# Kernel tuning notes

Hardware: AMD Instinct MI355X
Metric: run time of the kernel (lower is better)

## Reference

```python
import jax, jax.numpy as jnp
import numpy as np

B, T, D = 2, 1024, 768
H, HS = 12, 64          # n_head, head_size = n_embed // n_head
E, K = 8, 1             # num_experts, top-k (MoeLayer default k=1)
DF = 4 * D              # FFN hidden
EPS = 1e-5


def _ln(x, g, b):
    mu = jnp.mean(x, axis=-1, keepdims=True)
    var = jnp.mean(jnp.square(x - mu), axis=-1, keepdims=True)
    return (x - mu) * jax.lax.rsqrt(var + EPS) * g + b


def setup_inputs() -> dict:
    key = jax.random.key(0)
    ks = jax.random.split(key, 12)
    s = 0.02
    return {
        "x": jax.random.normal(ks[0], (B, T, D), dtype=jnp.float32),
        "ln1_g": jnp.ones((D,), jnp.float32),
        "ln1_b": jnp.zeros((D,), jnp.float32),
        "ln2_g": jnp.ones((D,), jnp.float32),
        "ln2_b": jnp.zeros((D,), jnp.float32),
        "Wq": jax.random.normal(ks[1], (H, D, HS), jnp.float32) * s,
        "Wk": jax.random.normal(ks[2], (H, D, HS), jnp.float32) * s,
        "Wv": jax.random.normal(ks[3], (H, D, HS), jnp.float32) * s,
        "Wp": jax.random.normal(ks[4], (D, D), jnp.float32) * s,
        "bp": jnp.zeros((D,), jnp.float32),
        "Wg": jax.random.normal(ks[5], (D, E), jnp.float32) * s,
        "W1": jax.random.normal(ks[6], (E, D, DF), jnp.float32) * s,
        "b1": jnp.zeros((E, DF), jnp.float32),
        "W2": jax.random.normal(ks[7], (E, DF, D), jnp.float32) * s,
        "b2": jnp.zeros((E, D), jnp.float32),
    }


def reference(x, ln1_g, ln1_b, ln2_g, ln2_b, Wq, Wk, Wv, Wp, bp, Wg, W1, b1, W2, b2):
    b, t, d = x.shape

    # ---- multi-head causal self-attention (per-head QKV, as in Head) ----
    h = _ln(x, ln1_g, ln1_b)
    q = jnp.einsum('btd,hds->bhts', h, Wq)
    k = jnp.einsum('btd,hds->bhts', h, Wk)
    v = jnp.einsum('btd,hds->bhts', h, Wv)
    # NOTE: original scales by C**-0.5 with C = n_embed (not head_size)
    scores = jnp.einsum('bhts,bhus->bhtu', q, k) * (d ** -0.5)
    causal = jnp.tril(jnp.ones((t, t), dtype=bool))
    scores = jnp.where(causal, scores, -jnp.inf)
    att = jax.nn.softmax(scores, axis=-1)
    out = jnp.einsum('bhtu,bhus->bhts', att, v)          # [B,H,T,HS]
    out = out.transpose(0, 2, 1, 3).reshape(b, t, d)     # concat heads
    x = x + out @ Wp + bp

    # ---- top-k MoE feed-forward (MoeLayer, k=1) ----
    h2 = _ln(x, ln2_g, ln2_b).reshape(-1, d)             # [N,D]
    gate_logits = h2 @ Wg                                # [N,E]
    w, sel = jax.lax.top_k(gate_logits, K)               # [N,K]
    w = jax.nn.softmax(w.astype(jnp.float32), axis=-1).astype(x.dtype)
    n = h2.shape[0]
    combine = jnp.zeros((n, Wg.shape[1]), x.dtype).at[
        jnp.arange(n)[:, None], sel].add(w)              # [N,E]
    hid = jax.nn.relu(jnp.einsum('nd,edf->enf', h2, W1) + b1[:, None, :])
    y = jnp.einsum('enf,efd->end', hid, W2) + b2[:, None, :]
    moe = jnp.einsum('ne,end->nd', combine, y)           # dense dispatch
    return x + moe.reshape(b, t, d)
```

## Files before the change

kernel.cpp:

```cpp
#include <hip/hip_runtime.h>
#include <math.h>

typedef __bf16 bf16;
typedef __bf16 bf16x4 __attribute__((ext_vector_type(4)));
typedef __bf16 bf16x8 __attribute__((ext_vector_type(8)));
typedef float f32x4 __attribute__((ext_vector_type(4)));

#define N_TOK 2048
#define DMODEL 768
#define NHEAD 12
#define TSEQ 1024
#define NEXP 8
#define DFF 3072

__device__ inline f32x4 mfma16(bf16x8 a, bf16x8 b, f32x4 c) {
    return __builtin_amdgcn_mfma_f32_16x16x32_bf16(a, b, c, 0, 0, 0);
}

__device__ inline f32x4 zero4() { f32x4 z = {0.f, 0.f, 0.f, 0.f}; return z; }

__device__ inline float block_sum(float v, float* red, int tid) {
#pragma unroll
    for (int off = 32; off > 0; off >>= 1) v += __shfl_down(v, off, 64);
    __syncthreads();
    if ((tid & 63) == 0) red[tid >> 6] = v;
    __syncthreads();
    return red[0] + red[1] + red[2] + red[3];
}

__global__ __launch_bounds__(256) void ln1_kernel(const float* __restrict__ x,
        const float* __restrict__ g, const float* __restrict__ b,
        bf16* __restrict__ hh, bf16* __restrict__ hl,
        int* __restrict__ cz, float* __restrict__ outz) {
    __shared__ float red[4];
    int row = blockIdx.x, tid = threadIdx.x;
    if (row == 0 && tid < 16) cz[tid] = 0;
#pragma unroll
    for (int i = 0; i < 3; i++) outz[(size_t)row * DMODEL + tid + i * 256] = 0.f;
    const float* xr = x + (size_t)row * DMODEL;
    float v[3];
#pragma unroll
    for (int i = 0; i < 3; i++) v[i] = xr[tid + i * 256];
    float s = block_sum(v[0] + v[1] + v[2], red, tid);
    float mu = s * (1.f / DMODEL);
    float q = 0.f;
#pragma unroll
    for (int i = 0; i < 3; i++) { float d = v[i] - mu; q += d * d; }
    q = block_sum(q, red, tid);
    float rstd = 1.0f / sqrtf(q * (1.f / DMODEL) + 1e-5f);
#pragma unroll
    for (int i = 0; i < 3; i++) {
        int d = tid + i * 256;
        float val = (v[i] - mu) * rstd * g[d] + b[d];
        bf16 hi = (bf16)val;
        hh[(size_t)row * DMODEL + d] = hi;
        hl[(size_t)row * DMODEL + d] = (bf16)(val - (float)hi);
    }
}

__device__ inline void gemm_step3(const bf16* lah, const bf16* lal,
                                  const bf16* lbh, const bf16* lbl,
                                  int wm, int wn, int row16, int quad,
                                  f32x4 acc[4][4]) {
    bf16x8 ah[4], al[4], bh[4], bl[4];
#pragma unroll
    for (int i = 0; i < 4; i++) {
        int ro = (wm * 64 + i * 16 + row16) * 40 + quad * 8;
        ah[i] = *(const bf16x8*)&lah[ro];
        al[i] = *(const bf16x8*)&lal[ro];
    }
#pragma unroll
    for (int i = 0; i < 4; i++) {
        int ro = (wn * 64 + i * 16 + row16) * 40 + quad * 8;
        bh[i] = *(const bf16x8*)&lbh[ro];
        bl[i] = *(const bf16x8*)&lbl[ro];
    }
#pragma unroll
    for (int mi = 0; mi < 4; mi++)
#pragma unroll
        for (int ni = 0; ni < 4; ni++) {
            acc[mi][ni] = mfma16(ah[mi], bh[ni], acc[mi][ni]);
            acc[mi][ni] = mfma16(ah[mi], bl[ni], acc[mi][ni]);
            acc[mi][ni] = mfma16(al[mi], bh[ni], acc[mi][ni]);
        }
}

__device__ inline void gemm_step1(const bf16* la, const bf16* lb, int wm, int wn,
                                  int row16, int quad, f32x4 acc[4][4]) {
    bf16x8 af[4], bfr[4];
#pragma unroll
    for (int i = 0; i < 4; i++)
        af[i] = *(const bf16x8*)&la[(wm * 64 + i * 16 + row16) * 40 + quad * 8];
#pragma unroll
    for (int i = 0; i < 4; i++)
        bfr[i] = *(const bf16x8*)&lb[(wn * 64 + i * 16 + row16) * 40 + quad * 8];
#pragma unroll
    for (int mi = 0; mi < 4; mi++)
#pragma unroll
        for (int ni = 0; ni < 4; ni++)
            acc[mi][ni] = mfma16(af[mi], bfr[ni], acc[mi][ni]);
}

#define TILE_E (128 * 40)

__device__ inline void wstore_hilo(bf16* lbh, bf16* lbl, int base, const float* wv) {
#pragma unroll
    for (int gq = 0; gq < 4; gq++) {
        bf16x4 ph, pl;
#pragma unroll
        for (int j = 0; j < 4; j++) {
            float v = wv[gq * 4 + j];
            bf16 hi = (bf16)v;
            ph[j] = hi;
            pl[j] = (bf16)(v - (float)hi);
        }
        *(bf16x4*)&lbh[base + gq * 4] = ph;
        *(bf16x4*)&lbl[base + gq * 4] = pl;
    }
}
__device__ inline void wstore1(bf16* lb, int base, const float* wv) {
#pragma unroll
    for (int gq = 0; gq < 4; gq++) {
        bf16x4 p;
#pragma unroll
        for (int j = 0; j < 4; j++) p[j] = (bf16)wv[gq * 4 + j];
        *(bf16x4*)&lb[base + gq * 4] = p;
    }
}

__global__ __launch_bounds__(256) void qkv_gemm(const bf16* __restrict__ hA_h,
        const bf16* __restrict__ hA_l,
        const float* __restrict__ Wq, const float* __restrict__ Wk,
        const float* __restrict__ Wv,
        bf16* __restrict__ qh, bf16* __restrict__ ql,
        bf16* __restrict__ kh, bf16* __restrict__ kl,
        bf16* __restrict__ vh, bf16* __restrict__ vl) {
    __shared__ alignas(16) bf16 lah[2 * TILE_E];
    __shared__ alignas(16) bf16 lal[2 * TILE_E];
    __shared__ alignas(16) bf16 lbh[2 * TILE_E];
    __shared__ alignas(16) bf16 lbl[2 * TILE_E];
    int tid = threadIdx.x;
    int m0 = blockIdx.y * 128;
    int nt = blockIdx.x;
    int sel = nt / 6;
    int n0 = (nt % 6) * 128;
    const float* W = (sel == 0) ? Wq : (sel == 1) ? Wk : Wv;
    bf16* obh = (sel == 0) ? qh : (sel == 1) ? kh : vh;
    bf16* obl = (sel == 0) ? ql : (sel == 1) ? kl : vl;
    int lane = tid & 63, w = tid >> 6, row16 = lane & 15, quad = lane >> 4;
    int wm = w >> 1, wn = w & 1;
    int r_a = tid >> 2, c_a = (tid & 3) << 3;
    int nW = tid & 127, kb16 = (tid >> 7) * 16;
    size_t wcol = (size_t)((n0 + nW) >> 6) * DMODEL * 64 + ((n0 + nW) & 63);
    int wbase = nW * 40 + kb16;
    f32x4 acc[4][4];
#pragma unroll
    for (int mi = 0; mi < 4; mi++)
#pragma unroll
        for (int ni = 0; ni < 4; ni++) acc[mi][ni] = zero4();
    const bf16* Ah = hA_h + (size_t)m0 * DMODEL;
    const bf16* Al = hA_l + (size_t)m0 * DMODEL;
    bf16x8 rAh0, rAh1, rAl0, rAl1;
    float wv[16];
    rAh0 = *(const bf16x8*)&Ah[(size_t)r_a * DMODEL + c_a];
    rAh1 = *(const bf16x8*)&Ah[(size_t)(r_a + 64) * DMODEL + c_a];
    rAl0 = *(const bf16x8*)&Al[(size_t)r_a * DMODEL + c_a];
    rAl1 = *(const bf16x8*)&Al[(size_t)(r_a + 64) * DMODEL + c_a];
#pragma unroll
    for (int i = 0; i < 16; i++) wv[i] = W[wcol + (size_t)(kb16 + i) * 64];
    *(bf16x8*)&lah[r_a * 40 + c_a] = rAh0;
    *(bf16x8*)&lah[(r_a + 64) * 40 + c_a] = rAh1;
    *(bf16x8*)&lal[r_a * 40 + c_a] = rAl0;
    *(bf16x8*)&lal[(r_a + 64) * 40 + c_a] = rAl1;
    wstore_hilo(lbh, lbl, wbase, wv);
    const int nk = DMODEL / 32;
    for (int ki = 0; ki < nk; ki++) {
        __syncthreads();
        int cur = (ki & 1) * TILE_E, nxt = ((ki + 1) & 1) * TILE_E;
        if (ki + 1 < nk) {
            int k0 = (ki + 1) * 32;
            rAh0 = *(const bf16x8*)&Ah[(size_t)r_a * DMODEL + k0 + c_a];
            rAh1 = *(const bf16x8*)&Ah[(size_t)(r_a + 64) * DMODEL + k0 + c_a];
            rAl0 = *(const bf16x8*)&Al[(size_t)r_a * DMODEL + k0 + c_a];
            rAl1 = *(const bf16x8*)&Al[(size_t)(r_a + 64) * DMODEL + k0 + c_a];
#pragma unroll
            for (int i = 0; i < 16; i++)
                wv[i] = W[wcol + (size_t)(k0 + kb16 + i) * 64];
        }
        gemm_step3(lah + cur, lal + cur, lbh + cur, lbl + cur, wm, wn, row16, quad, acc);
        if (ki + 1 < nk) {
            *(bf16x8*)&lah[nxt + r_a * 40 + c_a] = rAh0;
            *(bf16x8*)&lah[nxt + (r_a + 64) * 40 + c_a] = rAh1;
            *(bf16x8*)&lal[nxt + r_a * 40 + c_a] = rAl0;
            *(bf16x8*)&lal[nxt + (r_a + 64) * 40 + c_a] = rAl1;
            wstore_hilo(lbh + nxt, lbl + nxt, wbase, wv);
        }
    }
#pragma unroll
    for (int mi = 0; mi < 4; mi++) {
        int rowl = wm * 64 + mi * 16 + quad * 4;
#pragma unroll
        for (int ni = 0; ni < 4; ni++) {
            int col = n0 + wn * 64 + ni * 16 + row16;
            int hhd = col >> 6, s = col & 63;
#pragma unroll
            for (int r = 0; r < 4; r++) {
                int gm = m0 + rowl + r;
                int bb = gm >> 10, t = gm & 1023;
                size_t oi = (((size_t)bb * NHEAD + hhd) * TSEQ + t) * 64 + s;
                float val = acc[mi][ni][r];
                bf16 hi = (bf16)val;
                obh[oi] = hi;
                obl[oi] = (bf16)(val - (float)hi);
            }
        }
    }
}

__global__ __launch_bounds__(256) void attn_kernel(const bf16* __restrict__ qhb,
        const bf16* __restrict__ qlb, const bf16* __restrict__ khb,
        const bf16* __restrict__ klb, const bf16* __restrict__ vhb,
        const bf16* __restrict__ vlb, bf16* __restrict__ aoh,
        bf16* __restrict__ aol) {
    __shared__ alignas(16) bf16 kt_h[64 * 72];
    __shared__ alignas(16) bf16 kt_l[64 * 72];
    __shared__ alignas(16) bf16 vt_h[64 * 72];
    __shared__ alignas(16) bf16 vt_l[64 * 72];
    __shared__ alignas(16) bf16 p_h[4][16 * 72];
    __shared__ alignas(16) bf16 p_l[4][16 * 72];
    int qt = blockIdx.x, bh = blockIdx.y;
    int b = bh / NHEAD, hh = bh % NHEAD;
    int tid = threadIdx.x, lane = tid & 63, w = tid >> 6;
    int row16 = lane & 15, quad = lane >> 4;
    const bf16* qph = qhb + (size_t)bh * TSEQ * 64;
    const bf16* qpl = qlb + (size_t)bh * TSEQ * 64;
    const bf16* kph = khb + (size_t)bh * TSEQ * 64;
    const bf16* kpl = klb + (size_t)bh * TSEQ * 64;
    const bf16* vph = vhb + (size_t)bh * TSEQ * 64;
    const bf16* vpl = vlb + (size_t)bh * TSEQ * 64;
    int qrow = qt * 64 + w * 16 + row16;
    bf16x8 aq_h[2], aq_l[2];
#pragma unroll
    for (int kk = 0; kk < 2; kk++) {
        aq_h[kk] = *(const bf16x8*)&qph[(size_t)qrow * 64 + kk * 32 + quad * 8];
        aq_l[kk] = *(const bf16x8*)&qpl[(size_t)qrow * 64 + kk * 32 + quad * 8];
    }
    f32x4 o[4];
    float m_i[4], l_i[4];
#pragma unroll
    for (int i = 0; i < 4; i++) { o[i] = zero4(); m_i[i] = -INFINITY; l_i[i] = 0.f; }
    const float sc = 0.03608439182435161f;
    for (int kt = 0; kt <= qt; kt++) {
        __syncthreads();
#pragma unroll
        for (int i = 0; i < 2; i++) {
            int chunk = tid + i * 256;
            int r = chunk >> 3, c = (chunk & 7) << 3;
            size_t gi = (size_t)(kt * 64 + r) * 64 + c;
            *(bf16x8*)&kt_h[r * 72 + c] = *(const bf16x8*)&kph[gi];
            *(bf16x8*)&kt_l[r * 72 + c] = *(const bf16x8*)&kpl[gi];
        }
#pragma unroll
        for (int u = 0; u < 4; u++) {
            int unit = tid + u * 256;
            int s = unit & 63, tg = unit >> 6;
            bf16x4 ph, pl;
#pragma unroll
            for (int j = 0; j < 4; j++) {
                size_t gi = (size_t)(kt * 64 + tg * 4 + j) * 64 + s;
                ph[j] = vph[gi];
                pl[j] = vpl[gi];
            }
            *(bf16x4*)&vt_h[s * 72 + tg * 4] = ph;
            *(bf16x4*)&vt_l[s * 72 + tg * 4] = pl;
        }
        __syncthreads();
        f32x4 sacc[4];
#pragma unroll
        for (int ni = 0; ni < 4; ni++) {
            sacc[ni] = zero4();
#pragma unroll
            for (int kk = 0; kk < 2; kk++) {
                int ro = (ni * 16 + row16) * 72 + kk * 32 + quad * 8;
                bf16x8 bk_h = *(const bf16x8*)&kt_h[ro];
                bf16x8 bk_l = *(const bf16x8*)&kt_l[ro];
                sacc[ni] = mfma16(aq_h[kk], bk_h, sacc[ni]);
                sacc[ni] = mfma16(aq_h[kk], bk_l, sacc[ni]);
                sacc[ni] = mfma16(aq_l[kk], bk_h, sacc[ni]);
            }
        }
        float mrow[4];
#pragma unroll
        for (int r = 0; r < 4; r++) mrow[r] = -INFINITY;
        int tq_b = qt * 64 + w * 16 + quad * 4;
#pragma unroll
        for (int ni = 0; ni < 4; ni++) {
            int tkg = kt * 64 + ni * 16 + row16;
#pragma unroll
            for (int r = 0; r < 4; r++) {
                float sv = sacc[ni][r] * sc;
                if (tkg > tq_b + r) sv = -INFINITY;
                sacc[ni][r] = sv;
                mrow[r] = fmaxf(mrow[r], sv);
            }
        }
#pragma unroll
        for (int r = 0; r < 4; r++) {
#pragma unroll
            for (int off = 8; off > 0; off >>= 1)
                mrow[r] = fmaxf(mrow[r], __shfl_xor(mrow[r], off, 16));
        }
        float alpha[4], rsum[4];
#pragma unroll
        for (int r = 0; r < 4; r++) {
            float nm = fmaxf(m_i[r], mrow[r]);
            alpha[r] = __expf(m_i[r] - nm);
            m_i[r] = nm;
            rsum[r] = 0.f;
        }
#pragma unroll
        for (int ni = 0; ni < 4; ni++)
#pragma unroll
            for (int r = 0; r < 4; r++) {
                float p = __expf(sacc[ni][r] - m_i[r]);
                sacc[ni][r] = p;
                rsum[r] += p;
            }
#pragma unroll
        for (int r = 0; r < 4; r++) {
#pragma unroll
            for (int off = 8; off > 0; off >>= 1)
                rsum[r] += __shfl_xor(rsum[r], off, 16);
            l_i[r] = l_i[r] * alpha[r] + rsum[r];
        }
#pragma unroll
        for (int ni = 0; ni < 4; ni++)
#pragma unroll
            for (int r = 0; r < 4; r++) o[ni][r] *= alpha[r];
#pragma unroll
        for (int ni = 0; ni < 4; ni++)
#pragma unroll
            for (int r = 0; r < 4; r++) {
                float p = sacc[ni][r];
                bf16 hi = (bf16)p;
                int po = (quad * 4 + r) * 72 + ni * 16 + row16;
                p_h[w][po] = hi;
                p_l[w][po] = (bf16)(p - (float)hi);
            }
        __syncthreads();
        bf16x8 ap_h[2], ap_l[2];
#pragma unroll
        for (int kk = 0; kk < 2; kk++) {
            ap_h[kk] = *(const bf16x8*)&p_h[w][row16 * 72 + kk * 32 + quad * 8];
            ap_l[kk] = *(const bf16x8*)&p_l[w][row16 * 72 + kk * 32 + quad * 8];
        }
#pragma unroll
        for (int ni = 0; ni < 4; ni++)
#pragma unroll
            for (int kk = 0; kk < 2; kk++) {
                int ro = (ni * 16 + row16) * 72 + kk * 32 + quad * 8;
                bf16x8 bv_h = *(const bf16x8*)&vt_h[ro];
                bf16x8 bv_l = *(const bf16x8*)&vt_l[ro];
                o[ni] = mfma16(ap_h[kk], bv_h, o[ni]);
                o[ni] = mfma16(ap_h[kk], bv_l, o[ni]);
                o[ni] = mfma16(ap_l[kk], bv_h, o[ni]);
            }
    }
    int t = qt * 64 + w * 16 + quad * 4;
#pragma unroll
    for (int ni = 0; ni < 4; ni++) {
        int col = hh * 64 + ni * 16 + row16;
#pragma unroll
        for (int r = 0; r < 4; r++) {
            float val = o[ni][r] / l_i[r];
            size_t n = (size_t)b * TSEQ + t + r;
            bf16 hi = (bf16)val;
            aoh[n * DMODEL + col] = hi;
            aol[n * DMODEL + col] = (bf16)(val - (float)hi);
        }
    }
}

__global__ __launch_bounds__(256) void proj_gemm(const bf16* __restrict__ aInH,
        const bf16* __restrict__ aInL,
        const float* __restrict__ Wp, const float* __restrict__ bp,
        const float* __restrict__ x, float* __restrict__ x1) {
    __shared__ alignas(16) bf16 lah[2 * TILE_E];
    __shared__ alignas(16) bf16 lal[2 * TILE_E];
    __shared__ alignas(16) bf16 lbh[2 * TILE_E];
    __shared__ alignas(16) bf16 lbl[2 * TILE_E];
    int tid = threadIdx.x;
    int m0 = blockIdx.y * 128, n0 = blockIdx.x * 128;
    int lane = tid & 63, w = tid >> 6, row16 = lane & 15, quad = lane >> 4;
    int wm = w >> 1, wn = w & 1;
    int r_a = tid >> 2, c_a = (tid & 3) << 3;
    int nW = tid & 127, kb16 = (tid >> 7) * 16;
    int wbase = nW * 40 + kb16;
    f32x4 acc[4][4];
#pragma unroll
    for (int mi = 0; mi < 4; mi++)
#pragma unroll
        for (int ni = 0; ni < 4; ni++) acc[mi][ni] = zero4();
    const bf16* Ah = aInH + (size_t)m0 * DMODEL;
    const bf16* Al = aInL + (size_t)m0 * DMODEL;
    bf16x8 rAh0, rAh1, rAl0, rAl1;
    float wv[16];
    rAh0 = *(const bf16x8*)&Ah[(size_t)r_a * DMODEL + c_a];
    rAh1 = *(const bf16x8*)&Ah[(size_t)(r_a + 64) * DMODEL + c_a];
    rAl0 = *(const bf16x8*)&Al[(size_t)r_a * DMODEL + c_a];
    rAl1 = *(const bf16x8*)&Al[(size_t)(r_a + 64) * DMODEL + c_a];
#pragma unroll
    for (int i = 0; i < 16; i++)
        wv[i] = Wp[(size_t)(kb16 + i) * DMODEL + n0 + nW];
    *(bf16x8*)&lah[r_a * 40 + c_a] = rAh0;
    *(bf16x8*)&lah[(r_a + 64) * 40 + c_a] = rAh1;
    *(bf16x8*)&lal[r_a * 40 + c_a] = rAl0;
    *(bf16x8*)&lal[(r_a + 64) * 40 + c_a] = rAl1;
    wstore_hilo(lbh, lbl, wbase, wv);
    const int nk = DMODEL / 32;
    for (int ki = 0; ki < nk; ki++) {
        __syncthreads();
        int cur = (ki & 1) * TILE_E, nxt = ((ki + 1) & 1) * TILE_E;
        if (ki + 1 < nk) {
            int k0 = (ki + 1) * 32;
            rAh0 = *(const bf16x8*)&Ah[(size_t)r_a * DMODEL + k0 + c_a];
            rAh1 = *(const bf16x8*)&Ah[(size_t)(r_a + 64) * DMODEL + k0 + c_a];
            rAl0 = *(const bf16x8*)&Al[(size_t)r_a * DMODEL + k0 + c_a];
            rAl1 = *(const bf16x8*)&Al[(size_t)(r_a + 64) * DMODEL + k0 + c_a];
#pragma unroll
            for (int i = 0; i < 16; i++)
                wv[i] = Wp[(size_t)(k0 + kb16 + i) * DMODEL + n0 + nW];
        }
        gemm_step3(lah + cur, lal + cur, lbh + cur, lbl + cur, wm, wn, row16, quad, acc);
        if (ki + 1 < nk) {
            *(bf16x8*)&lah[nxt + r_a * 40 + c_a] = rAh0;
            *(bf16x8*)&lah[nxt + (r_a + 64) * 40 + c_a] = rAh1;
            *(bf16x8*)&lal[nxt + r_a * 40 + c_a] = rAl0;
            *(bf16x8*)&lal[nxt + (r_a + 64) * 40 + c_a] = rAl1;
            wstore_hilo(lbh + nxt, lbl + nxt, wbase, wv);
        }
    }
#pragma unroll
    for (int mi = 0; mi < 4; mi++) {
        int rowl = wm * 64 + mi * 16 + quad * 4;
#pragma unroll
        for (int ni = 0; ni < 4; ni++) {
            int col = n0 + wn * 64 + ni * 16 + row16;
#pragma unroll
            for (int r = 0; r < 4; r++) {
                int gm = m0 + rowl + r;
                x1[(size_t)gm * DMODEL + col] =
                    acc[mi][ni][r] + bp[col] + x[(size_t)gm * DMODEL + col];
            }
        }
    }
}

__global__ __launch_bounds__(256) void ln2_gate_kernel(const float* __restrict__ x1,
        const float* __restrict__ g, const float* __restrict__ b,
        const float* __restrict__ Wg, bf16* __restrict__ h2,
        int* __restrict__ sel, int* __restrict__ counts) {
    __shared__ float red[4];
    __shared__ float glog[8];
    int row = blockIdx.x, tid = threadIdx.x;
    if (tid < 8) glog[tid] = 0.f;
    const float* xr = x1 + (size_t)row * DMODEL;
    float v[3];
#pragma unroll
    for (int i = 0; i < 3; i++) v[i] = xr[tid + i * 256];
    float s = block_sum(v[0] + v[1] + v[2], red, tid);
    float mu = s * (1.f / DMODEL);
    float qv = 0.f;
#pragma unroll
    for (int i = 0; i < 3; i++) { float d = v[i] - mu; qv += d * d; }
    qv = block_sum(qv, red, tid);
    float rstd = 1.0f / sqrtf(qv * (1.f / DMODEL) + 1e-5f);
    float ga[8];
#pragma unroll
    for (int e = 0; e < 8; e++) ga[e] = 0.f;
#pragma unroll
    for (int i = 0; i < 3; i++) {
        int d = tid + i * 256;
        float hv = (v[i] - mu) * rstd * g[d] + b[d];
        h2[(size_t)row * DMODEL + d] = (bf16)hv;
        const float* wgr = Wg + (size_t)d * NEXP;
#pragma unroll
        for (int e = 0; e < 8; e++) ga[e] += hv * wgr[e];
    }
#pragma unroll
    for (int e = 0; e < 8; e++)
#pragma unroll
        for (int off = 32; off > 0; off >>= 1) ga[e] += __shfl_down(ga[e], off, 64);
    if ((tid & 63) == 0)
#pragma unroll
        for (int e = 0; e < 8; e++) atomicAdd(&glog[e], ga[e]);
    __syncthreads();
    if (tid == 0) {
        float best = glog[0];
        int bi = 0;
#pragma unroll
        for (int e = 1; e < 8; e++)
            if (glog[e] > best) { best = glog[e]; bi = e; }
        sel[row] = bi;
        atomicAdd(&counts[bi], 1);
    }
}

__global__ void scatter_kernel(const int* __restrict__ sel, const int* __restrict__ counts,
                               int* __restrict__ cursor, int* __restrict__ perm) {
    int n = blockIdx.x * blockDim.x + threadIdx.x;
    if (n >= N_TOK) return;
    int e = sel[n];
    int off = 0;
    for (int i = 0; i < NEXP; i++) off += (i < e) ? counts[i] : 0;
    int pos = atomicAdd(&cursor[e], 1);
    perm[off + pos] = n;
}

__global__ __launch_bounds__(256) void moe1_gemm(const bf16* __restrict__ h2,
        const float* __restrict__ W1, const float* __restrict__ b1,
        const int* __restrict__ counts, const int* __restrict__ perm,
        bf16* __restrict__ hid) {
    int e = blockIdx.z;
    int cnt = counts[e];
    int rt = blockIdx.y;
    if (rt * 128 >= cnt) return;
    int off = 0;
    for (int i = 0; i < NEXP; i++) off += (i < e) ? counts[i] : 0;
    int n0 = blockIdx.x * 128;
    const float* W = W1 + (size_t)e * DMODEL * DFF;
    __shared__ alignas(16) bf16 la[2 * TILE_E];
    __shared__ alignas(16) bf16 lb[2 * TILE_E];
    int tid = threadIdx.x;
    int lane = tid & 63, w = tid >> 6, row16 = lane & 15, quad = lane >> 4;
    int wm = w >> 1, wn = w & 1;
    int r_a = tid >> 2, c_a = (tid & 3) << 3;
    int nW = tid & 127, kb16 = (tid >> 7) * 16;
    int wbase = nW * 40 + kb16;
    int tok0 = perm[off + min(rt * 128 + r_a, cnt - 1)];
    int tok1 = perm[off + min(rt * 128 + r_a + 64, cnt - 1)];
    const bf16* a0 = h2 + (size_t)tok0 * DMODEL;
    const bf16* a1 = h2 + (size_t)tok1 * DMODEL;
    f32x4 acc[4][4];
#pragma unroll
    for (int mi = 0; mi < 4; mi++)
#pragma unroll
        for (int ni = 0; ni < 4; ni++) acc[mi][ni] = zero4();
    bf16x8 rA0, rA1;
    float wv[16];
    rA0 = *(const bf16x8*)&a0[c_a];
    rA1 = *(const bf16x8*)&a1[c_a];
#pragma unroll
    for (int i = 0; i < 16; i++)
        wv[i] = W[(size_t)(kb16 + i) * DFF + n0 + nW];
    *(bf16x8*)&la[r_a * 40 + c_a] = rA0;
    *(bf16x8*)&la[(r_a + 64) * 40 + c_a] = rA1;
    wstore1(lb, wbase, wv);
    const int nk = DMODEL / 32;
    for (int ki = 0; ki < nk; ki++) {
        __syncthreads();
        int cur = (ki & 1) * TILE_E, nxt = ((ki + 1) & 1) * TILE_E;
        if (ki + 1 < nk) {
            int k0 = (ki + 1) * 32;
            rA0 = *(const bf16x8*)&a0[k0 + c_a];
            rA1 = *(const bf16x8*)&a1[k0 + c_a];
#pragma unroll
            for (int i = 0; i < 16; i++)
                wv[i] = W[(size_t)(k0 + kb16 + i) * DFF + n0 + nW];
        }
        gemm_step1(la + cur, lb + cur, wm, wn, row16, quad, acc);
        if (ki + 1 < nk) {
            *(bf16x8*)&la[nxt + r_a * 40 + c_a] = rA0;
            *(bf16x8*)&la[nxt + (r_a + 64) * 40 + c_a] = rA1;
            wstore1(lb + nxt, wbase, wv);
        }
    }
#pragma unroll
    for (int mi = 0; mi < 4; mi++) {
        int rowl = wm * 64 + mi * 16 + quad * 4;
#pragma unroll
        for (int ni = 0; ni < 4; ni++) {
            int col = n0 + wn * 64 + ni * 16 + row16;
#pragma unroll
            for (int r = 0; r < 4; r++) {
                int lr = rowl + r;
                if (rt * 128 + lr < cnt) {
                    float val = acc[mi][ni][r] + b1[(size_t)e * DFF + col];
                    val = fmaxf(val, 0.f);
                    hid[(size_t)(off + rt * 128 + lr) * DFF + col] = (bf16)val;
                }
            }
        }
    }
}

__global__ __launch_bounds__(256) void moe2_gemm(const bf16* __restrict__ hid,
        const float* __restrict__ W2, const float* __restrict__ b2,
        const int* __restrict__ counts, const int* __restrict__ perm,
        const float* __restrict__ x1, float* __restrict__ out) {
    int ez = blockIdx.z;
    int e = ez & 7, ks = ez >> 3;
    int cnt = counts[e];
    int rt = blockIdx.y;
    if (rt * 128 >= cnt) return;
    int off = 0;
    for (int i = 0; i < NEXP; i++) off += (i < e) ? counts[i] : 0;
    int n0 = blockIdx.x * 128;
    const float* W = W2 + (size_t)e * DFF * DMODEL;
    __shared__ alignas(16) bf16 la[2 * TILE_E];
    __shared__ alignas(16) bf16 lb[2 * TILE_E];
    int tid = threadIdx.x;
    int lane = tid & 63, w = tid >> 6, row16 = lane & 15, quad = lane >> 4;
    int wm = w >> 1, wn = w & 1;
    int r_a = tid >> 2, c_a = (tid & 3) << 3;
    int nW = tid & 127, kb16 = (tid >> 7) * 16;
    int wbase = nW * 40 + kb16;
    const bf16* a0 = hid + (size_t)min(off + rt * 128 + r_a, N_TOK - 1) * DFF;
    const bf16* a1 = hid + (size_t)min(off + rt * 128 + r_a + 64, N_TOK - 1) * DFF;
    f32x4 acc[4][4];
#pragma unroll
    for (int mi = 0; mi < 4; mi++)
#pragma unroll
        for (int ni = 0; ni < 4; ni++) acc[mi][ni] = zero4();
    const int kst = ks * (DFF / 4);
    bf16x8 rA0, rA1;
    float wv[16];
    rA0 = *(const bf16x8*)&a0[kst + c_a];
    rA1 = *(const bf16x8*)&a1[kst + c_a];
#pragma unroll
    for (int i = 0; i < 16; i++)
        wv[i] = W[(size_t)(kst + kb16 + i) * DMODEL + n0 + nW];
    *(bf16x8*)&la[r_a * 40 + c_a] = rA0;
    *(bf16x8*)&la[(r_a + 64) * 40 + c_a] = rA1;
    wstore1(lb, wbase, wv);
    const int nk = (DFF / 4) / 32;
    for (int ki = 0; ki < nk; ki++) {
        __syncthreads();
        int cur = (ki & 1) * TILE_E, nxt = ((ki + 1) & 1) * TILE_E;
        if (ki + 1 < nk) {
            int k0 = kst + (ki + 1) * 32;
            rA0 = *(const bf16x8*)&a0[k0 + c_a];
            rA1 = *(const bf16x8*)&a1[k0 + c_a];
#pragma unroll
            for (int i = 0; i < 16; i++)
                wv[i] = W[(size_t)(k0 + kb16 + i) * DMODEL + n0 + nW];
        }
        gemm_step1(la + cur, lb + cur, wm, wn, row16, quad, acc);
        if (ki + 1 < nk) {
            *(bf16x8*)&la[nxt + r_a * 40 + c_a] = rA0;
            *(bf16x8*)&la[nxt + (r_a + 64) * 40 + c_a] = rA1;
            wstore1(lb + nxt, wbase, wv);
        }
    }
#pragma unroll
    for (int mi = 0; mi < 4; mi++) {
        int rowl = wm * 64 + mi * 16 + quad * 4;
#pragma unroll
        for (int ni = 0; ni < 4; ni++) {
            int col = n0 + wn * 64 + ni * 16 + row16;
#pragma unroll
            for (int r = 0; r < 4; r++) {
                int lr = rowl + r;
                if (rt * 128 + lr < cnt) {
                    int n = perm[off + rt * 128 + lr];
                    float val = acc[mi][ni][r];
                    if (ks == 0)
                        val += b2[(size_t)e * DMODEL + col] + x1[(size_t)n * DMODEL + col];
                    atomicAdd(&out[(size_t)n * DMODEL + col], val);
                }
            }
        }
    }
}

extern "C" void kernel_launch(void* const* d_in, const int* in_sizes, int n_in,
                              void* d_out, int out_size, void* d_ws, size_t ws_size,
                              hipStream_t stream) {
    const float* x    = (const float*)d_in[0];
    const float* ln1g = (const float*)d_in[1];
    const float* ln1b = (const float*)d_in[2];
    const float* ln2g = (const float*)d_in[3];
    const float* ln2b = (const float*)d_in[4];
    const float* Wq   = (const float*)d_in[5];
    const float* Wk   = (const float*)d_in[6];
    const float* Wv   = (const float*)d_in[7];
    const float* Wp   = (const float*)d_in[8];
    const float* bp   = (const float*)d_in[9];
    const float* Wg   = (const float*)d_in[10];
    const float* W1   = (const float*)d_in[11];
    const float* b1   = (const float*)d_in[12];
    const float* W2   = (const float*)d_in[13];
    const float* b2   = (const float*)d_in[14];
    float* out = (float*)d_out;

    char* ws = (char*)d_ws;
    size_t off = 0;
    const size_t SZ = (size_t)N_TOK * DMODEL * 2;
    bf16* h1h = (bf16*)(ws + off); off += SZ;
    bf16* h1l = (bf16*)(ws + off); off += SZ;
    bf16* qh  = (bf16*)(ws + off); off += SZ;
    bf16* ql  = (bf16*)(ws + off); off += SZ;
    bf16* kh  = (bf16*)(ws + off); off += SZ;
    bf16* kl  = (bf16*)(ws + off); off += SZ;
    bf16* vh  = (bf16*)(ws + off); off += SZ;
    bf16* vl  = (bf16*)(ws + off); off += SZ;
    bf16* aoh = (bf16*)(ws + off); off += SZ;
    bf16* aol = (bf16*)(ws + off); off += SZ;
    float* x1 = (float*)(ws + off); off += (size_t)N_TOK * DMODEL * 4;
    bf16* h2  = (bf16*)(ws + off); off += SZ;
    bf16* hid = (bf16*)(ws + off); off += (size_t)N_TOK * DFF * 2;
    int* counts  = (int*)(ws + off); off += 8 * 4;
    int* cursor  = (int*)(ws + off); off += 8 * 4;
    int* sel     = (int*)(ws + off); off += (size_t)N_TOK * 4;
    int* perm    = (int*)(ws + off); off += (size_t)N_TOK * 4;

    ln1_kernel<<<N_TOK, 256, 0, stream>>>(x, ln1g, ln1b, h1h, h1l, counts, out);
    qkv_gemm<<<dim3(18, 16), 256, 0, stream>>>(h1h, h1l, Wq, Wk, Wv, qh, ql, kh, kl, vh, vl);
    attn_kernel<<<dim3(16, 24), 256, 0, stream>>>(qh, ql, kh, kl, vh, vl, aoh, aol);
    proj_gemm<<<dim3(6, 16), 256, 0, stream>>>(aoh, aol, Wp, bp, x, x1);
    ln2_gate_kernel<<<N_TOK, 256, 0, stream>>>(x1, ln2g, ln2b, Wg, h2, sel, counts);
    scatter_kernel<<<8, 256, 0, stream>>>(sel, counts, cursor, perm);
    moe1_gemm<<<dim3(24, 16, 8), 256, 0, stream>>>(h2, W1, b1, counts, perm, hid);
    moe2_gemm<<<dim3(6, 16, 32), 256, 0, stream>>>(hid, W2, b2, counts, perm, x1, out);
}
```

Before: 511.8 us.

## Prefetch two K tiles ahead in GEMMs and flatten grids to 1D

Restructures the qkv, proj, moe1 and moe2 GEMM main loops to hold two register stages of global loads, so each tile is fetched two K-steps before it is consumed. The loop is unrolled by two over the LDS double buffer. The qkv, proj and moe2 grids are flattened to a 1D launch padded to a power-of-two stride, and the padded blocks return early. The aim is to hide more global-load latency, at the cost of higher register pressure and some wasted idle blocks.

```diff
diff --git a/kernel.cpp b/kernel.cpp
--- a/kernel.cpp
+++ b/kernel.cpp
@@ -139,9 +139,11 @@
     __shared__ alignas(16) bf16 lal[2 * TILE_E];
     __shared__ alignas(16) bf16 lbh[2 * TILE_E];
     __shared__ alignas(16) bf16 lbl[2 * TILE_E];
+    int id = blockIdx.x;
+    int nt = id % 24;
+    if (nt >= 18) return;
+    int m0 = (id / 24) * 128;
     int tid = threadIdx.x;
-    int m0 = blockIdx.y * 128;
-    int nt = blockIdx.x;
     int sel = nt / 6;
     int n0 = (nt % 6) * 128;
     const float* W = (sel == 0) ? Wq : (sel == 1) ? Wk : Wv;
@@ -160,42 +162,42 @@
         for (int ni = 0; ni < 4; ni++) acc[mi][ni] = zero4();
     const bf16* Ah = hA_h + (size_t)m0 * DMODEL;
     const bf16* Al = hA_l + (size_t)m0 * DMODEL;
-    bf16x8 rAh0, rAh1, rAl0, rAl1;
-    float wv[16];
-    rAh0 = *(const bf16x8*)&Ah[(size_t)r_a * DMODEL + c_a];
-    rAh1 = *(const bf16x8*)&Ah[(size_t)(r_a + 64) * DMODEL + c_a];
-    rAl0 = *(const bf16x8*)&Al[(size_t)r_a * DMODEL + c_a];
-    rAl1 = *(const bf16x8*)&Al[(size_t)(r_a + 64) * DMODEL + c_a];
-#pragma unroll
-    for (int i = 0; i < 16; i++) wv[i] = W[wcol + (size_t)(kb16 + i) * 64];
-    *(bf16x8*)&lah[r_a * 40 + c_a] = rAh0;
-    *(bf16x8*)&lah[(r_a + 64) * 40 + c_a] = rAh1;
-    *(bf16x8*)&lal[r_a * 40 + c_a] = rAl0;
-    *(bf16x8*)&lal[(r_a + 64) * 40 + c_a] = rAl1;
-    wstore_hilo(lbh, lbl, wbase, wv);
+    bf16x8 rAh0_0, rAh1_0, rAl0_0, rAl1_0, rAh0_1, rAh1_1, rAl0_1, rAl1_1;
+    float wv0[16], wv1[16];
+
+#define QK_LOAD(bk, k0) do { \
+    rAh0_##bk = *(const bf16x8*)&Ah[(size_t)r_a * DMODEL + (k0) + c_a]; \
+    rAh1_##bk = *(const bf16x8*)&Ah[(size_t)(r_a + 64) * DMODEL + (k0) + c_a]; \
+    rAl0_##bk = *(const bf16x8*)&Al[(size_t)r_a * DMODEL + (k0) + c_a]; \
+    rAl1_##bk = *(const bf16x8*)&Al[(size_t)(r_a + 64) * DMODEL + (k0) + c_a]; \
+    _Pragma("unroll") for (int i = 0; i < 16; i++) \
+        wv##bk[i] = W[wcol + (size_t)((k0) + kb16 + i) * 64]; \
+} while (0)
+#define QK_STORE(bk, lofs) do { \
+    *(bf16x8*)&lah[(lofs) + r_a * 40 + c_a] = rAh0_##bk; \
+    *(bf16x8*)&lah[(lofs) + (r_a + 64) * 40 + c_a] = rAh1_##bk; \
+    *(bf16x8*)&lal[(lofs) + r_a * 40 + c_a] = rAl0_##bk; \
+    *(bf16x8*)&lal[(lofs) + (r_a + 64) * 40 + c_a] = rAl1_##bk; \
+    wstore_hilo(lbh + (lofs), lbl + (lofs), wbase, wv##bk); \
+} while (0)
+
     const int nk = DMODEL / 32;
-    for (int ki = 0; ki < nk; ki++) {
-        __syncthreads();
-        int cur = (ki & 1) * TILE_E, nxt = ((ki + 1) & 1) * TILE_E;
-        if (ki + 1 < nk) {
-            int k0 = (ki + 1) * 32;
-            rAh0 = *(const bf16x8*)&Ah[(size_t)r_a * DMODEL + k0 + c_a];
-            rAh1 = *(const bf16x8*)&Ah[(size_t)(r_a + 64) * DMODEL + k0 + c_a];
-            rAl0 = *(const bf16x8*)&Al[(size_t)r_a * DMODEL + k0 + c_a];
-            rAl1 = *(const bf16x8*)&Al[(size_t)(r_a + 64) * DMODEL + k0 + c_a];
-#pragma unroll
-            for (int i = 0; i < 16; i++)
-                wv[i] = W[wcol + (size_t)(k0 + kb16 + i) * 64];
-        }
-        gemm_step3(lah + cur, lal + cur, lbh + cur, lbl + cur, wm, wn, row16, quad, acc);
-        if (ki + 1 < nk) {
-            *(bf16x8*)&lah[nxt + r_a * 40 + c_a] = rAh0;
-            *(bf16x8*)&lah[nxt + (r_a + 64) * 40 + c_a] = rAh1;
-            *(bf16x8*)&lal[nxt + r_a * 40 + c_a] = rAl0;
-            *(bf16x8*)&lal[nxt + (r_a + 64) * 40 + c_a] = rAl1;
-            wstore_hilo(lbh + nxt, lbl + nxt, wbase, wv);
-        }
-    }
+    QK_LOAD(0, 0);
+    QK_LOAD(1, 32);
+    QK_STORE(0, 0);
+    for (int ki = 0; ki < nk; ki += 2) {
+        __syncthreads();
+        if (ki + 2 < nk) QK_LOAD(0, (ki + 2) * 32);
+        gemm_step3(lah, lal, lbh, lbl, wm, wn, row16, quad, acc);
+        QK_STORE(1, TILE_E);
+        __syncthreads();
+        if (ki + 3 < nk) QK_LOAD(1, (ki + 3) * 32);
+        gemm_step3(lah + TILE_E, lal + TILE_E, lbh + TILE_E, lbl + TILE_E,
+                   wm, wn, row16, quad, acc);
+        if (ki + 2 < nk) QK_STORE(0, 0);
+    }
+#undef QK_LOAD
+#undef QK_STORE
 #pragma unroll
     for (int mi = 0; mi < 4; mi++) {
         int rowl = wm * 64 + mi * 16 + quad * 4;
@@ -389,8 +391,11 @@
     __shared__ alignas(16) bf16 lal[2 * TILE_E];
     __shared__ alignas(16) bf16 lbh[2 * TILE_E];
     __shared__ alignas(16) bf16 lbl[2 * TILE_E];
+    int id = blockIdx.x;
+    int n0t = id & 7;
+    if (n0t >= 6) return;
+    int m0 = (id >> 3) * 128, n0 = n0t * 128;
     int tid = threadIdx.x;
-    int m0 = blockIdx.y * 128, n0 = blockIdx.x * 128;
     int lane = tid & 63, w = tid >> 6, row16 = lane & 15, quad = lane >> 4;
     int wm = w >> 1, wn = w & 1;
     int r_a = tid >> 2, c_a = (tid & 3) << 3;
@@ -403,43 +408,42 @@
         for (int ni = 0; ni < 4; ni++) acc[mi][ni] = zero4();
     const bf16* Ah = aInH + (size_t)m0 * DMODEL;
     const bf16* Al = aInL + (size_t)m0 * DMODEL;
-    bf16x8 rAh0, rAh1, rAl0, rAl1;
-    float wv[16];
-    rAh0 = *(const bf16x8*)&Ah[(size_t)r_a * DMODEL + c_a];
-    rAh1 = *(const bf16x8*)&Ah[(size_t)(r_a + 64) * DMODEL + c_a];
-    rAl0 = *(const bf16x8*)&Al[(size_t)r_a * DMODEL + c_a];
-    rAl1 = *(const bf16x8*)&Al[(size_t)(r_a + 64) * DMODEL + c_a];
-#pragma unroll
-    for (int i = 0; i < 16; i++)
-        wv[i] = Wp[(size_t)(kb16 + i) * DMODEL + n0 + nW];
-    *(bf16x8*)&lah[r_a * 40 + c_a] = rAh0;
-    *(bf16x8*)&lah[(r_a + 64) * 40 + c_a] = rAh1;
-    *(bf16x8*)&lal[r_a * 40 + c_a] = rAl0;
-    *(bf16x8*)&lal[(r_a + 64) * 40 + c_a] = rAl1;
-    wstore_hilo(lbh, lbl, wbase, wv);
+    bf16x8 rAh0_0, rAh1_0, rAl0_0, rAl1_0, rAh0_1, rAh1_1, rAl0_1, rAl1_1;
+    float wv0[16], wv1[16];
+
+#define PJ_LOAD(bk, k0) do { \
+    rAh0_##bk = *(const bf16x8*)&Ah[(size_t)r_a * DMODEL + (k0) + c_a]; \
+    rAh1_##bk = *(const bf16x8*)&Ah[(size_t)(r_a + 64) * DMODEL + (k0) + c_a]; \
+    rAl0_##bk = *(const bf16x8*)&Al[(size_t)r_a * DMODEL + (k0) + c_a]; \
+    rAl1_##bk = *(const bf16x8*)&Al[(size_t)(r_a + 64) * DMODEL + (k0) + c_a]; \
+    _Pragma("unroll") for (int i = 0; i < 16; i++) \
+        wv##bk[i] = Wp[(size_t)((k0) + kb16 + i) * DMODEL + n0 + nW]; \
+} while (0)
+#define PJ_STORE(bk, lofs) do { \
+    *(bf16x8*)&lah[(lofs) + r_a * 40 + c_a] = rAh0_##bk; \
+    *(bf16x8*)&lah[(lofs) + (r_a + 64) * 40 + c_a] = rAh1_##bk; \
+    *(bf16x8*)&lal[(lofs) + r_a * 40 + c_a] = rAl0_##bk; \
+    *(bf16x8*)&lal[(lofs) + (r_a + 64) * 40 + c_a] = rAl1_##bk; \
+    wstore_hilo(lbh + (lofs), lbl + (lofs), wbase, wv##bk); \
+} while (0)
+
     const int nk = DMODEL / 32;
-    for (int ki = 0; ki < nk; ki++) {
-        __syncthreads();
-        int cur = (ki & 1) * TILE_E, nxt = ((ki + 1) & 1) * TILE_E;
-        if (ki + 1 < nk) {
-            int k0 = (ki + 1) * 32;
-            rAh0 = *(const bf16x8*)&Ah[(size_t)r_a * DMODEL + k0 + c_a];
-            rAh1 = *(const bf16x8*)&Ah[(size_t)(r_a + 64) * DMODEL + k0 + c_a];
-            rAl0 = *(const bf16x8*)&Al[(size_t)r_a * DMODEL + k0 + c_a];
-            rAl1 = *(const bf16x8*)&Al[(size_t)(r_a + 64) * DMODEL + k0 + c_a];
-#pragma unroll
-            for (int i = 0; i < 16; i++)
-                wv[i] = Wp[(size_t)(k0 + kb16 + i) * DMODEL + n0 + nW];
-        }
-        gemm_step3(lah + cur, lal + cur, lbh + cur, lbl + cur, wm, wn, row16, quad, acc);
-        if (ki + 1 < nk) {
-            *(bf16x8*)&lah[nxt + r_a * 40 + c_a] = rAh0;
-            *(bf16x8*)&lah[nxt + (r_a + 64) * 40 + c_a] = rAh1;
-            *(bf16x8*)&lal[nxt + r_a * 40 + c_a] = rAl0;
-            *(bf16x8*)&lal[nxt + (r_a + 64) * 40 + c_a] = rAl1;
-            wstore_hilo(lbh + nxt, lbl + nxt, wbase, wv);
-        }
-    }
+    PJ_LOAD(0, 0);
+    PJ_LOAD(1, 32);
+    PJ_STORE(0, 0);
+    for (int ki = 0; ki < nk; ki += 2) {
+        __syncthreads();
+        if (ki + 2 < nk) PJ_LOAD(0, (ki + 2) * 32);
+        gemm_step3(lah, lal, lbh, lbl, wm, wn, row16, quad, acc);
+        PJ_STORE(1, TILE_E);
+        __syncthreads();
+        if (ki + 3 < nk) PJ_LOAD(1, (ki + 3) * 32);
+        gemm_step3(lah + TILE_E, lal + TILE_E, lbh + TILE_E, lbl + TILE_E,
+                   wm, wn, row16, quad, acc);
+        if (ki + 2 < nk) PJ_STORE(0, 0);
+    }
+#undef PJ_LOAD
+#undef PJ_STORE
 #pragma unroll
     for (int mi = 0; mi < 4; mi++) {
         int rowl = wm * 64 + mi * 16 + quad * 4;
@@ -546,35 +550,37 @@
     for (int mi = 0; mi < 4; mi++)
 #pragma unroll
         for (int ni = 0; ni < 4; ni++) acc[mi][ni] = zero4();
-    bf16x8 rA0, rA1;
-    float wv[16];
-    rA0 = *(const bf16x8*)&a0[c_a];
-    rA1 = *(const bf16x8*)&a1[c_a];
-#pragma unroll
-    for (int i = 0; i < 16; i++)
-        wv[i] = W[(size_t)(kb16 + i) * DFF + n0 + nW];
-    *(bf16x8*)&la[r_a * 40 + c_a] = rA0;
-    *(bf16x8*)&la[(r_a + 64) * 40 + c_a] = rA1;
-    wstore1(lb, wbase, wv);
+    bf16x8 rA0_0, rA1_0, rA0_1, rA1_1;
+    float wv0[16], wv1[16];
+
+#define M1_LOAD(bk, k0) do { \
+    rA0_##bk = *(const bf16x8*)&a0[(k0) + c_a]; \
+    rA1_##bk = *(const bf16x8*)&a1[(k0) + c_a]; \
+    _Pragma("unroll") for (int i = 0; i < 16; i++) \
+        wv##bk[i] = W[(size_t)((k0) + kb16 + i) * DFF + n0 + nW]; \
+} while (0)
+#define M1_STORE(bk, lofs) do { \
+    *(bf16x8*)&la[(lofs) + r_a * 40 + c_a] = rA0_##bk; \
+    *(bf16x8*)&la[(lofs) + (r_a + 64) * 40 + c_a] = rA1_##bk; \
+    wstore1(lb + (lofs), wbase, wv##bk); \
+} while (0)
+
     const int nk = DMODEL / 32;
-    for (int ki = 0; ki < nk; ki++) {
-        __syncthreads();
-        int cur = (ki & 1) * TILE_E, nxt = ((ki + 1) & 1) * TILE_E;
-        if (ki + 1 < nk) {
-            int k0 = (ki + 1) * 32;
-            rA0 = *(const bf16x8*)&a0[k0 + c_a];
-            rA1 = *(const bf16x8*)&a1[k0 + c_a];
-#pragma unroll
-            for (int i = 0; i < 16; i++)
-                wv[i] = W[(size_t)(k0 + kb16 + i) * DFF + n0 + nW];
-        }
-        gemm_step1(la + cur, lb + cur, wm, wn, row16, quad, acc);
-        if (ki + 1 < nk) {
-            *(bf16x8*)&la[nxt + r_a * 40 + c_a] = rA0;
-            *(bf16x8*)&la[nxt + (r_a + 64) * 40 + c_a] = rA1;
-            wstore1(lb + nxt, wbase, wv);
-        }
-    }
+    M1_LOAD(0, 0);
+    M1_LOAD(1, 32);
+    M1_STORE(0, 0);
+    for (int ki = 0; ki < nk; ki += 2) {
+        __syncthreads();
+        if (ki + 2 < nk) M1_LOAD(0, (ki + 2) * 32);
+        gemm_step1(la, lb, wm, wn, row16, quad, acc);
+        M1_STORE(1, TILE_E);
+        __syncthreads();
+        if (ki + 3 < nk) M1_LOAD(1, (ki + 3) * 32);
+        gemm_step1(la + TILE_E, lb + TILE_E, wm, wn, row16, quad, acc);
+        if (ki + 2 < nk) M1_STORE(0, 0);
+    }
+#undef M1_LOAD
+#undef M1_STORE
 #pragma unroll
     for (int mi = 0; mi < 4; mi++) {
         int rowl = wm * 64 + mi * 16 + quad * 4;
@@ -598,14 +604,17 @@
         const float* __restrict__ W2, const float* __restrict__ b2,
         const int* __restrict__ counts, const int* __restrict__ perm,
         const float* __restrict__ x1, float* __restrict__ out) {
-    int ez = blockIdx.z;
+    int id = blockIdx.x;
+    int n0t = id & 7;
+    if (n0t >= 6) return;
+    int rt = (id >> 3) & 15;
+    int ez = id >> 7;
     int e = ez & 7, ks = ez >> 3;
     int cnt = counts[e];
-    int rt = blockIdx.y;
     if (rt * 128 >= cnt) return;
     int off = 0;
     for (int i = 0; i < NEXP; i++) off += (i < e) ? counts[i] : 0;
-    int n0 = blockIdx.x * 128;
+    int n0 = n0t * 128;
     const float* W = W2 + (size_t)e * DFF * DMODEL;
     __shared__ alignas(16) bf16 la[2 * TILE_E];
     __shared__ alignas(16) bf16 lb[2 * TILE_E];
@@ -615,43 +624,46 @@
     int r_a = tid >> 2, c_a = (tid & 3) << 3;
     int nW = tid & 127, kb16 = (tid >> 7) * 16;
     int wbase = nW * 40 + kb16;
-    const bf16* a0 = hid + (size_t)min(off + rt * 128 + r_a, N_TOK - 1) * DFF;
-    const bf16* a1 = hid + (size_t)min(off + rt * 128 + r_a + 64, N_TOK - 1) * DFF;
+    const int kst = ks * (DFF / 4);
+    const bf16* a0 = hid + (size_t)min(off + rt * 128 + r_a, N_TOK - 1) * DFF + kst;
+    const bf16* a1 = hid + (size_t)min(off + rt * 128 + r_a + 64, N_TOK - 1) * DFF + kst;
+    const float* Wk_ = W + (size_t)kst * DMODEL;
     f32x4 acc[4][4];
 #pragma unroll
     for (int mi = 0; mi < 4; mi++)
 #pragma unroll
         for (int ni = 0; ni < 4; ni++) acc[mi][ni] = zero4();
-    const int kst = ks * (DFF / 4);
-    bf16x8 rA0, rA1;
-    float wv[16];
-    rA0 = *(const bf16x8*)&a0[kst + c_a];
-    rA1 = *(const bf16x8*)&a1[kst + c_a];
-#pragma unroll
-    for (int i = 0; i < 16; i++)
-        wv[i] = W[(size_t)(kst + kb16 + i) * DMODEL + n0 + nW];
-    *(bf16x8*)&la[r_a * 40 + c_a] = rA0;
-    *(bf16x8*)&la[(r_a + 64) * 40 + c_a] = rA1;
-    wstore1(lb, wbase, wv);
+    bf16x8 rA0_0, rA1_0, rA0_1, rA1_1;
+    float wv0[16], wv1[16];
+
+#define M2_LOAD(bk, k0) do { \
+    rA0_##bk = *(const bf16x8*)&a0[(k0) + c_a]; \
+    rA1_##bk = *(const bf16x8*)&a1[(k0) + c_a]; \
+    _Pragma("unroll") for (int i = 0; i < 16; i++) \
+        wv##bk[i] = Wk_[(size_t)((k0) + kb16 + i) * DMODEL + n0 + nW]; \
+} while (0)
+#define M2_STORE(bk, lofs) do { \
+    *(bf16x8*)&la[(lofs) + r_a * 40 + c_a] = rA0_##bk; \
+    *(bf16x8*)&la[(lofs) + (r_a + 64) * 40 + c_a] = rA1_##bk; \
+    wstore1(lb + (lofs), wbase, wv##bk); \
+} while (0)
+
     const int nk = (DFF / 4) / 32;
-    for (int ki = 0; ki < nk; ki++) {
-        __syncthreads();
-        int cur = (ki & 1) * TILE_E, nxt = ((ki + 1) & 1) * TILE_E;
-        if (ki + 1 < nk) {
-            int k0 = kst + (ki + 1) * 32;
-            rA0 = *(const bf16x8*)&a0[k0 + c_a];
-            rA1 = *(const bf16x8*)&a1[k0 + c_a];
-#pragma unroll
-            for (int i = 0; i < 16; i++)
-                wv[i] = W[(size_t)(k0 + kb16 + i) * DMODEL + n0 + nW];
-        }
-        gemm_step1(la + cur, lb + cur, wm, wn, row16, quad, acc);
-        if (ki + 1 < nk) {
-            *(bf16x8*)&la[nxt + r_a * 40 + c_a] = rA0;
-            *(bf16x8*)&la[nxt + (r_a + 64) * 40 + c_a] = rA1;
-            wstore1(lb + nxt, wbase, wv);
-        }
-    }
+    M2_LOAD(0, 0);
+    M2_LOAD(1, 32);
+    M2_STORE(0, 0);
+    for (int ki = 0; ki < nk; ki += 2) {
+        __syncthreads();
+        if (ki + 2 < nk) M2_LOAD(0, (ki + 2) * 32);
+        gemm_step1(la, lb, wm, wn, row16, quad, acc);
+        M2_STORE(1, TILE_E);
+        __syncthreads();
+        if (ki + 3 < nk) M2_LOAD(1, (ki + 3) * 32);
+        gemm_step1(la + TILE_E, lb + TILE_E, wm, wn, row16, quad, acc);
+        if (ki + 2 < nk) M2_STORE(0, 0);
+    }
+#undef M2_LOAD
+#undef M2_STORE
 #pragma unroll
     for (int mi = 0; mi < 4; mi++) {
         int rowl = wm * 64 + mi * 16 + quad * 4;
@@ -715,11 +727,11 @@
     int* perm    = (int*)(ws + off); off += (size_t)N_TOK * 4;
 
     ln1_kernel<<<N_TOK, 256, 0, stream>>>(x, ln1g, ln1b, h1h, h1l, counts, out);
-    qkv_gemm<<<dim3(18, 16), 256, 0, stream>>>(h1h, h1l, Wq, Wk, Wv, qh, ql, kh, kl, vh, vl);
+    qkv_gemm<<<24 * 16, 256, 0, stream>>>(h1h, h1l, Wq, Wk, Wv, qh, ql, kh, kl, vh, vl);
     attn_kernel<<<dim3(16, 24), 256, 0, stream>>>(qh, ql, kh, kl, vh, vl, aoh, aol);
-    proj_gemm<<<dim3(6, 16), 256, 0, stream>>>(aoh, aol, Wp, bp, x, x1);
+    proj_gemm<<<8 * 16, 256, 0, stream>>>(aoh, aol, Wp, bp, x, x1);
     ln2_gate_kernel<<<N_TOK, 256, 0, stream>>>(x1, ln2g, ln2b, Wg, h2, sel, counts);
     scatter_kernel<<<8, 256, 0, stream>>>(sel, counts, cursor, perm);
     moe1_gemm<<<dim3(24, 16, 8), 256, 0, stream>>>(h2, W1, b1, counts, perm, hid);
-    moe2_gemm<<<dim3(6, 16, 32), 256, 0, stream>>>(hid, W2, b2, counts, perm, x1, out);
-}
+    moe2_gemm<<<8 * 16 * 32, 256, 0, stream>>>(hid, W2, b2, counts, perm, x1, out);
+}
```

After: 625.5 us. 22.2% more time.
